# Performance work log

Hardware: AMD Instinct MI355X
Metric: run time of the kernel (lower is better)

The kernel has to match this reference:

```python
import jax, jax.numpy as jnp
import numpy as np

WIN = (8, 8)        # window height, width
HEADS = 6
DIM = 192
HEAD_DIM = DIM // HEADS
SCALE = HEAD_DIM ** -0.5
ALPHA = 0.2         # leaky_relu negative slope (tf.nn.leaky_relu / keras default)


def _leaky(t):
    return jnp.where(t >= 0, t, ALPHA * t)


def _relative_position_index():
    # Faithful to the TF code: tf.meshgrid defaults to 'xy' indexing.
    wh, ww = WIN
    mh, mw = jnp.meshgrid(jnp.arange(wh), jnp.arange(ww))  # each [ww, wh] (xy)
    coords = jnp.stack([mh, mw])                           # [2, ww, wh]
    flat = coords.reshape(2, -1)                           # [2, N]
    rel = flat[:, :, None] - flat[:, None, :]              # [2, N, N]
    rel = jnp.transpose(rel, (1, 2, 0))                    # [N, N, 2]
    idx = (rel[:, :, 0] + wh - 1) * (2 * ww - 1) + (rel[:, :, 1] + ww - 1)
    return idx                                             # [N, N] int32


def setup_inputs() -> dict:
    key = jax.random.key(0)
    ks = jax.random.split(key, 6)
    B_, N, C = 4096, WIN[0] * WIN[1], DIM
    std = 0.02
    return {
        "x": jax.random.normal(ks[0], (B_, N, C), dtype=jnp.float32),
        "wq": jax.random.normal(ks[1], (C, C), dtype=jnp.float32) * (C ** -0.5),
        "bq": jnp.zeros((C,), dtype=jnp.float32),
        "wkv": jax.random.normal(ks[2], (C, 2 * C), dtype=jnp.float32) * (C ** -0.5),
        "bkv": jnp.zeros((2 * C,), dtype=jnp.float32),
        "bias_table": jax.random.normal(ks[3], ((2 * WIN[0] - 1) * (2 * WIN[1] - 1), HEADS), dtype=jnp.float32) * std,
        "proj_w": jax.random.normal(ks[4], (C, C), dtype=jnp.float32) * (C ** -0.5),
        "proj_b": jnp.zeros((C,), dtype=jnp.float32),
    }


def reference(x, wq, bq, wkv, bkv, bias_table, proj_w, proj_b):
    B_, N, C = x.shape
    H, D = HEADS, HEAD_DIM

    # QKV projections with LeakyReLU activation (as in LinearProjection)
    q = _leaky(x @ wq + bq).reshape(B_, N, H, D).transpose(0, 2, 1, 3)      # [B,H,N,D]
    kv = _leaky(x @ wkv + bkv).reshape(B_, N, 2, H, D).transpose(2, 0, 3, 1, 4)
    k, v = kv[0], kv[1]                                                      # [B,H,N,D]

    # scaled attention scores
    attn = jnp.einsum('bhnd,bhmd->bhnm', q * SCALE, k)                       # [B,H,N,N]

    # gathered relative position bias (ratio == 1 here, tf.repeat is no-op)
    idx = _relative_position_index()                                         # [N,N]
    bias = bias_table[idx]                                                   # [N,N,H]
    attn = attn + jnp.transpose(bias, (2, 0, 1))[None]                       # [B,H,N,N]

    attn = jax.nn.softmax(attn, axis=-1)
    out = jnp.einsum('bhnm,bhmd->bhnd', attn, v)                             # [B,H,N,D]
    out = out.transpose(0, 2, 1, 3).reshape(B_, N, C)
    return out @ proj_w + proj_b
```

## Files before the change

kernel.cpp:

```cpp
#include <hip/hip_runtime.h>
#include <hip/hip_bf16.h>

typedef __bf16 bf16;
typedef bf16 bf16x8 __attribute__((ext_vector_type(8)));
typedef bf16 bf16x4 __attribute__((ext_vector_type(4)));
typedef short s16x4 __attribute__((ext_vector_type(4)));
typedef float f32x4 __attribute__((ext_vector_type(4)));

#define SCALE 0.17677669529663687f

#define XSTR 208
#define SMEM_ELEMS 13312

#if defined(__has_builtin)
#if __has_builtin(__builtin_amdgcn_mfma_f32_16x16x16bf16_1k)
#define HAS_MFMA16 1
#endif
#endif

__global__ void wattn_prep(const float* __restrict__ wq, const float* __restrict__ wkv,
                           const float* __restrict__ bias_table, const float* __restrict__ proj_w,
                           bf16* __restrict__ wqkvT, bf16* __restrict__ projT,
                           float* __restrict__ biasB)
{
    int t = blockIdx.x * 256 + threadIdx.x;
    if (t < 110592) {
        int n = t / 192, k = t % 192;
        float v = (n < 192) ? wq[k * 192 + n] : wkv[k * 384 + (n - 192)];
        wqkvT[t] = (bf16)v;
    } else if (t < 147456) {
        int e = t - 110592;
        int n = e / 192, k = e % 192;
        projT[e] = (bf16)proj_w[k * 192 + n];
    } else if (t < 172032) {
        int e = t - 147456;
        int h  = e >> 12;
        int mb = (e >> 8) & 15;
        int n  = (e >> 2) & 63;
        int mr = e & 3;
        int m  = mb * 4 + mr;
        int idx = ((n & 7) - (m & 7) + 7) * 15 + ((n >> 3) - (m >> 3) + 7);
        biasB[e] = bias_table[idx * 6 + h];
    }
}

#if !defined(HAS_MFMA16)
__device__ __forceinline__ bf16x8 build8(bf16x4 t0, bf16x4 t1, int li, int gi) {
    union { bf16x4 v; unsigned u[2]; } a0, a1;
    a0.v = t0; a1.v = t1;
    int b = li + 32 * (gi & 1);
    unsigned l0  = __shfl(a0.u[0], b),      l1  = __shfl(a0.u[1], b);
    unsigned l0h = __shfl(a0.u[0], b + 16), l1h = __shfl(a0.u[1], b + 16);
    unsigned h0  = __shfl(a1.u[0], b),      h1  = __shfl(a1.u[1], b);
    unsigned h0h = __shfl(a1.u[0], b + 16), h1h = __shfl(a1.u[1], b + 16);
    bool hi = (gi & 2);
    union { bf16x8 v8; unsigned u[4]; } r;
    r.u[0] = hi ? h0 : l0;   r.u[1] = hi ? h1 : l1;
    r.u[2] = hi ? h0h : l0h; r.u[3] = hi ? h1h : l1h;
    return r.v8;
}
#endif

__global__ __launch_bounds__(384, 4)
void wattn_main(const float* __restrict__ x, const bf16* __restrict__ wqkvT,
                const float* __restrict__ bq, const float* __restrict__ bkv,
                const bf16* __restrict__ projT, const float* __restrict__ biasB,
                const float* __restrict__ proj_b, float* __restrict__ outg)
{
    __shared__ __align__(16) bf16 smem[SMEM_ELEMS];
    const int tid = threadIdx.x;
    const int li  = tid & 15;
    const int gi  = (tid >> 4) & 3;
    const int w   = tid >> 6;
    const int win = blockIdx.x;

    bf16* xb = smem;
    const int srow = tid / 48, scol = tid % 48;
    const f32x4 fz = {0.f, 0.f, 0.f, 0.f};

    {
        const float4* xg = (const float4*)(x + (size_t)win * 12288);
#pragma unroll
        for (int i = 0; i < 8; ++i) {
            float4 p = xg[(srow + 8 * i) * 48 + scol];
            bf16x4 v; v[0]=(bf16)p.x; v[1]=(bf16)p.y; v[2]=(bf16)p.z; v[3]=(bf16)p.w;
            *(bf16x4*)&xb[(srow + 8 * i) * XSTR + scol * 4] = v;
        }
    }
    __syncthreads();

    bf16x4 qf[2][4], kf[2][4];
    {
        f32x4 bjq0 = *(const f32x4*)&bq [32 * w + 4 * gi];
        f32x4 bjq1 = *(const f32x4*)&bq [32 * w + 16 + 4 * gi];
        f32x4 bjk0 = *(const f32x4*)&bkv[32 * w + 4 * gi];
        f32x4 bjk1 = *(const f32x4*)&bkv[32 * w + 16 + 4 * gi];
        f32x4 aqk[4][4];
#pragma unroll
        for (int c = 0; c < 4; ++c) {
            aqk[0][c] = bjq0; aqk[1][c] = bjq1;
            aqk[2][c] = bjk0; aqk[3][c] = bjk1;
        }
#pragma unroll 2
        for (int kk = 0; kk < 6; ++kk) {
            bf16x8 bx[4], aw[4];
#pragma unroll
            for (int c = 0; c < 4; ++c)
                bx[c] = *(const bf16x8*)&xb[(c * 16 + li) * XSTR + kk * 32 + gi * 8];
#pragma unroll
            for (int j = 0; j < 4; ++j) {
                int T = (j < 2) ? (2 * w + j) : (12 + 2 * w + (j - 2));
                aw[j] = *(const bf16x8*)&wqkvT[(size_t)(T * 16 + li) * 192 + kk * 32 + gi * 8];
            }
#pragma unroll
            for (int j = 0; j < 4; ++j)
#pragma unroll
                for (int c = 0; c < 4; ++c)
                    aqk[j][c] = __builtin_amdgcn_mfma_f32_16x16x32_bf16(aw[j], bx[c], aqk[j][c], 0, 0, 0);
        }
#pragma unroll
        for (int j = 0; j < 2; ++j)
#pragma unroll
            for (int c = 0; c < 4; ++c) {
                bf16x4 rq, rk;
#pragma unroll
                for (int rg = 0; rg < 4; ++rg) {
                    float tq = aqk[j][c][rg];
                    float tk = aqk[2 + j][c][rg];
                    tq = (fmaxf(tq, 0.f) + 0.2f * fminf(tq, 0.f)) * SCALE;
                    tk =  fmaxf(tk, 0.f) + 0.2f * fminf(tk, 0.f);
                    rq[rg] = (bf16)tq;
                    rk[rg] = (bf16)tk;
                }
                qf[j][c] = rq;
                kf[j][c] = rk;
            }
    }

    f32x4 s[4][4];
#pragma unroll
    for (int cm = 0; cm < 4; ++cm)
#pragma unroll
        for (int cn = 0; cn < 4; ++cn) {
            f32x4 bv = *(const f32x4*)&biasB[w * 4096 + (4 * cm + gi) * 256 + (16 * cn + li) * 4];
#if defined(HAS_MFMA16)
            f32x4 t = __builtin_amdgcn_mfma_f32_16x16x16bf16_1k(
                __builtin_bit_cast(s16x4, kf[0][cm]), __builtin_bit_cast(s16x4, qf[0][cn]), bv, 0, 0, 0);
            s[cm][cn] = __builtin_amdgcn_mfma_f32_16x16x16bf16_1k(
                __builtin_bit_cast(s16x4, kf[1][cm]), __builtin_bit_cast(s16x4, qf[1][cn]), t, 0, 0, 0);
#else
            s[cm][cn] = __builtin_amdgcn_mfma_f32_16x16x32_bf16(
                build8(kf[0][cm], kf[1][cm], li, gi), build8(qf[0][cn], qf[1][cn], li, gi), bv, 0, 0, 0);
#endif
        }

    float rs[4];
    bf16x4 pb[4][4];
#pragma unroll
    for (int cn = 0; cn < 4; ++cn) {
        float m_ = -1e30f;
#pragma unroll
        for (int cm = 0; cm < 4; ++cm)
#pragma unroll
            for (int rg = 0; rg < 4; ++rg) m_ = fmaxf(m_, s[cm][cn][rg]);
        m_ = fmaxf(m_, __shfl_xor(m_, 16));
        m_ = fmaxf(m_, __shfl_xor(m_, 32));
        float ss = 0.f;
#pragma unroll
        for (int cm = 0; cm < 4; ++cm) {
            bf16x4 r;
#pragma unroll
            for (int rg = 0; rg < 4; ++rg) {
                float p = __expf(s[cm][cn][rg] - m_);
                ss += p;
                r[rg] = (bf16)p;
            }
            pb[cm][cn] = r;
        }
        ss += __shfl_xor(ss, 16);
        ss += __shfl_xor(ss, 32);
        rs[cn] = 1.f / ss;
    }

    bf16x4 vf[2][4];
    {
        f32x4 bjv0 = *(const f32x4*)&bkv[192 + 32 * w + 4 * gi];
        f32x4 bjv1 = *(const f32x4*)&bkv[192 + 32 * w + 16 + 4 * gi];
        f32x4 av_[4][2];
#pragma unroll
        for (int rt = 0; rt < 4; ++rt) { av_[rt][0] = bjv0; av_[rt][1] = bjv1; }
#pragma unroll 2
        for (int kk = 0; kk < 6; ++kk) {
            bf16x8 a[4], bwv[2];
#pragma unroll
            for (int rt = 0; rt < 4; ++rt)
                a[rt] = *(const bf16x8*)&xb[(rt * 16 + li) * XSTR + kk * 32 + gi * 8];
#pragma unroll
            for (int j = 0; j < 2; ++j)
                bwv[j] = *(const bf16x8*)&wqkvT[(size_t)((24 + 2 * w + j) * 16 + li) * 192 + kk * 32 + gi * 8];
#pragma unroll
            for (int rt = 0; rt < 4; ++rt)
#pragma unroll
                for (int j = 0; j < 2; ++j)
                    av_[rt][j] = __builtin_amdgcn_mfma_f32_16x16x32_bf16(a[rt], bwv[j], av_[rt][j], 0, 0, 0);
        }
#pragma unroll
        for (int j = 0; j < 2; ++j)
#pragma unroll
            for (int rt = 0; rt < 4; ++rt) {
                bf16x4 r;
#pragma unroll
                for (int rg = 0; rg < 4; ++rg) {
                    float t = av_[rt][j][rg];
                    t = fmaxf(t, 0.f) + 0.2f * fminf(t, 0.f);
                    r[rg] = (bf16)t;
                }
                vf[j][rt] = r;
            }
    }

    f32x4 o[2][4];
#pragma unroll
    for (int ct = 0; ct < 2; ++ct)
#pragma unroll
        for (int cn = 0; cn < 4; ++cn) {
#if defined(HAS_MFMA16)
            f32x4 t = fz;
#pragma unroll
            for (int rt = 0; rt < 4; ++rt)
                t = __builtin_amdgcn_mfma_f32_16x16x16bf16_1k(
                        __builtin_bit_cast(s16x4, vf[ct][rt]),
                        __builtin_bit_cast(s16x4, pb[rt][cn]), t, 0, 0, 0);
            o[ct][cn] = t;
#else
            f32x4 t = fz;
#pragma unroll
            for (int c = 0; c < 2; ++c)
                t = __builtin_amdgcn_mfma_f32_16x16x32_bf16(
                        build8(vf[ct][2 * c], vf[ct][2 * c + 1], li, gi),
                        build8(pb[2 * c][cn], pb[2 * c + 1][cn], li, gi), t, 0, 0, 0);
            o[ct][cn] = t;
#endif
        }
    __syncthreads();

#pragma unroll
    for (int ct = 0; ct < 2; ++ct)
#pragma unroll
        for (int cn = 0; cn < 4; ++cn) {
            bf16x4 r;
#pragma unroll
            for (int rg = 0; rg < 4; ++rg) r[rg] = (bf16)(o[ct][cn][rg] * rs[cn]);
            *(bf16x4*)&xb[(cn * 16 + li) * XSTR + 32 * w + 16 * ct + 4 * gi] = r;
        }
    __syncthreads();

    f32x4 pa[2][4];
    {
        f32x4 pb0 = *(const f32x4*)&proj_b[32 * w + 4 * gi];
        f32x4 pb1 = *(const f32x4*)&proj_b[32 * w + 16 + 4 * gi];
#pragma unroll
        for (int cn = 0; cn < 4; ++cn) { pa[0][cn] = pb0; pa[1][cn] = pb1; }
    }
#pragma unroll 2
    for (int kk = 0; kk < 6; ++kk) {
        bf16x8 bo[4], awp[2];
#pragma unroll
        for (int cn = 0; cn < 4; ++cn)
            bo[cn] = *(const bf16x8*)&xb[(cn * 16 + li) * XSTR + kk * 32 + gi * 8];
#pragma unroll
        for (int ct = 0; ct < 2; ++ct)
            awp[ct] = *(const bf16x8*)&projT[(size_t)((2 * w + ct) * 16 + li) * 192 + kk * 32 + gi * 8];
#pragma unroll
        for (int ct = 0; ct < 2; ++ct)
#pragma unroll
            for (int cn = 0; cn < 4; ++cn)
                pa[ct][cn] = __builtin_amdgcn_mfma_f32_16x16x32_bf16(awp[ct], bo[cn], pa[ct][cn], 0, 0, 0);
    }

    {
        const int L = tid & 63;
        const int src = (L >> 2) + 16 * (L & 3);
        f32x4* og = (f32x4*)(outg + (size_t)win * 12288);
#pragma unroll
        for (int cn = 0; cn < 4; ++cn)
#pragma unroll
            for (int ct = 0; ct < 2; ++ct) {
                f32x4 y;
#pragma unroll
                for (int e = 0; e < 4; ++e)
                    y[e] = __shfl(pa[ct][cn][e], src);
                og[(16 * cn + (L >> 2)) * 48 + 8 * w + 4 * ct + (L & 3)] = y;
            }
    }
}

extern "C" void kernel_launch(void* const* d_in, const int* in_sizes, int n_in,
                              void* d_out, int out_size, void* d_ws, size_t ws_size,
                              hipStream_t stream)
{
    const float* x          = (const float*)d_in[0];
    const float* wq         = (const float*)d_in[1];
    const float* bq         = (const float*)d_in[2];
    const float* wkv        = (const float*)d_in[3];
    const float* bkv        = (const float*)d_in[4];
    const float* bias_table = (const float*)d_in[5];
    const float* proj_w     = (const float*)d_in[6];
    const float* proj_b     = (const float*)d_in[7];
    float* out = (float*)d_out;

    int B = in_sizes[0] / (64 * 192);

    bf16*  wqkvT = (bf16*)d_ws;
    bf16*  projT = (bf16*)((char*)d_ws + 221184);
    float* biasB = (float*)((char*)d_ws + 294912);

    wattn_prep<<<672, 256, 0, stream>>>(wq, wkv, bias_table, proj_w, wqkvT, projT, biasB);

    wattn_main<<<B, 384, 0, stream>>>(x, wqkvT, bq, bkv, projT, biasB, proj_b, out);
}
```

Before: 241.8 us.

## Process two windows per block with double-buffered x prefetch and MFMA priority

```diff
diff --git a/kernel.cpp b/kernel.cpp
--- a/kernel.cpp
+++ b/kernel.cpp
@@ -10,7 +10,8 @@
 #define SCALE 0.17677669529663687f
 
 #define XSTR 208
-#define SMEM_ELEMS 13312
+#define XELEMS 13312
+#define SMEM_ELEMS 26624
 
 #if defined(__has_builtin)
 #if __has_builtin(__builtin_amdgcn_mfma_f32_16x16x16bf16_1k)
@@ -65,233 +66,270 @@
 void wattn_main(const float* __restrict__ x, const bf16* __restrict__ wqkvT,
                 const float* __restrict__ bq, const float* __restrict__ bkv,
                 const bf16* __restrict__ projT, const float* __restrict__ biasB,
-                const float* __restrict__ proj_b, float* __restrict__ outg)
+                const float* __restrict__ proj_b, float* __restrict__ outg, int B)
 {
     __shared__ __align__(16) bf16 smem[SMEM_ELEMS];
     const int tid = threadIdx.x;
     const int li  = tid & 15;
     const int gi  = (tid >> 4) & 3;
     const int w   = tid >> 6;
-    const int win = blockIdx.x;
-
-    bf16* xb = smem;
+    const int win0 = blockIdx.x * 2;
+    if (win0 >= B) return;
+
     const int srow = tid / 48, scol = tid % 48;
     const f32x4 fz = {0.f, 0.f, 0.f, 0.f};
 
     {
-        const float4* xg = (const float4*)(x + (size_t)win * 12288);
-#pragma unroll
-        for (int i = 0; i < 8; ++i) {
-            float4 p = xg[(srow + 8 * i) * 48 + scol];
+        const float4* xg = (const float4*)(x + (size_t)win0 * 12288);
+#pragma unroll
+        for (int t = 0; t < 8; ++t) {
+            float4 p = xg[(srow + 8 * t) * 48 + scol];
             bf16x4 v; v[0]=(bf16)p.x; v[1]=(bf16)p.y; v[2]=(bf16)p.z; v[3]=(bf16)p.w;
-            *(bf16x4*)&xb[(srow + 8 * i) * XSTR + scol * 4] = v;
+            *(bf16x4*)&smem[(srow + 8 * t) * XSTR + scol * 4] = v;
         }
     }
     __syncthreads();
 
-    bf16x4 qf[2][4], kf[2][4];
-    {
-        f32x4 bjq0 = *(const f32x4*)&bq [32 * w + 4 * gi];
-        f32x4 bjq1 = *(const f32x4*)&bq [32 * w + 16 + 4 * gi];
-        f32x4 bjk0 = *(const f32x4*)&bkv[32 * w + 4 * gi];
-        f32x4 bjk1 = *(const f32x4*)&bkv[32 * w + 16 + 4 * gi];
-        f32x4 aqk[4][4];
-#pragma unroll
-        for (int c = 0; c < 4; ++c) {
-            aqk[0][c] = bjq0; aqk[1][c] = bjq1;
-            aqk[2][c] = bjk0; aqk[3][c] = bjk1;
-        }
+    int cur = 0;
+#pragma unroll 1
+    for (int i = 0; i < 2; ++i) {
+        const int win = win0 + i;
+        if (win >= B) break;
+        bf16* xb = smem + cur * XELEMS;
+        const bool pf = (i == 0) && (win0 + 1 < B);
+
+        bf16x4 qf[2][4], kf[2][4];
+        {
+            f32x4 bjq0 = *(const f32x4*)&bq [32 * w + 4 * gi];
+            f32x4 bjq1 = *(const f32x4*)&bq [32 * w + 16 + 4 * gi];
+            f32x4 bjk0 = *(const f32x4*)&bkv[32 * w + 4 * gi];
+            f32x4 bjk1 = *(const f32x4*)&bkv[32 * w + 16 + 4 * gi];
+            f32x4 aqk[4][4];
+#pragma unroll
+            for (int c = 0; c < 4; ++c) {
+                aqk[0][c] = bjq0; aqk[1][c] = bjq1;
+                aqk[2][c] = bjk0; aqk[3][c] = bjk1;
+            }
+            __builtin_amdgcn_s_setprio(1);
+#pragma unroll 2
+            for (int kk = 0; kk < 6; ++kk) {
+                bf16x8 bx[4], aw[4];
+#pragma unroll
+                for (int c = 0; c < 4; ++c)
+                    bx[c] = *(const bf16x8*)&xb[(c * 16 + li) * XSTR + kk * 32 + gi * 8];
+#pragma unroll
+                for (int j = 0; j < 4; ++j) {
+                    int T = (j < 2) ? (2 * w + j) : (12 + 2 * w + (j - 2));
+                    aw[j] = *(const bf16x8*)&wqkvT[(size_t)(T * 16 + li) * 192 + kk * 32 + gi * 8];
+                }
+#pragma unroll
+                for (int j = 0; j < 4; ++j)
+#pragma unroll
+                    for (int c = 0; c < 4; ++c)
+                        aqk[j][c] = __builtin_amdgcn_mfma_f32_16x16x32_bf16(aw[j], bx[c], aqk[j][c], 0, 0, 0);
+            }
+            __builtin_amdgcn_s_setprio(0);
+#pragma unroll
+            for (int j = 0; j < 2; ++j)
+#pragma unroll
+                for (int c = 0; c < 4; ++c) {
+                    bf16x4 rq, rk;
+#pragma unroll
+                    for (int rg = 0; rg < 4; ++rg) {
+                        float tq = aqk[j][c][rg];
+                        float tk = aqk[2 + j][c][rg];
+                        tq = (fmaxf(tq, 0.f) + 0.2f * fminf(tq, 0.f)) * SCALE;
+                        tk =  fmaxf(tk, 0.f) + 0.2f * fminf(tk, 0.f);
+                        rq[rg] = (bf16)tq;
+                        rk[rg] = (bf16)tk;
+                    }
+                    qf[j][c] = rq;
+                    kf[j][c] = rk;
+                }
+        }
+
+        f32x4 s[4][4];
+        __builtin_amdgcn_s_setprio(1);
+#pragma unroll
+        for (int cm = 0; cm < 4; ++cm)
+#pragma unroll
+            for (int cn = 0; cn < 4; ++cn) {
+                f32x4 bv = *(const f32x4*)&biasB[w * 4096 + (4 * cm + gi) * 256 + (16 * cn + li) * 4];
+#if defined(HAS_MFMA16)
+                f32x4 t = __builtin_amdgcn_mfma_f32_16x16x16bf16_1k(
+                    __builtin_bit_cast(s16x4, kf[0][cm]), __builtin_bit_cast(s16x4, qf[0][cn]), bv, 0, 0, 0);
+                s[cm][cn] = __builtin_amdgcn_mfma_f32_16x16x16bf16_1k(
+                    __builtin_bit_cast(s16x4, kf[1][cm]), __builtin_bit_cast(s16x4, qf[1][cn]), t, 0, 0, 0);
+#else
+                s[cm][cn] = __builtin_amdgcn_mfma_f32_16x16x32_bf16(
+                    build8(kf[0][cm], kf[1][cm], li, gi), build8(qf[0][cn], qf[1][cn], li, gi), bv, 0, 0, 0);
+#endif
+            }
+        __builtin_amdgcn_s_setprio(0);
+
+        float rs[4];
+        bf16x4 pb[4][4];
+#pragma unroll
+        for (int cn = 0; cn < 4; ++cn) {
+            float m_ = -1e30f;
+#pragma unroll
+            for (int cm = 0; cm < 4; ++cm)
+#pragma unroll
+                for (int rg = 0; rg < 4; ++rg) m_ = fmaxf(m_, s[cm][cn][rg]);
+            m_ = fmaxf(m_, __shfl_xor(m_, 16));
+            m_ = fmaxf(m_, __shfl_xor(m_, 32));
+            float ss = 0.f;
+#pragma unroll
+            for (int cm = 0; cm < 4; ++cm) {
+                bf16x4 r;
+#pragma unroll
+                for (int rg = 0; rg < 4; ++rg) {
+                    float p = __expf(s[cm][cn][rg] - m_);
+                    ss += p;
+                    r[rg] = (bf16)p;
+                }
+                pb[cm][cn] = r;
+            }
+            ss += __shfl_xor(ss, 16);
+            ss += __shfl_xor(ss, 32);
+            rs[cn] = 1.f / ss;
+        }
+
+        bf16x4 vf[2][4];
+        {
+            f32x4 bjv0 = *(const f32x4*)&bkv[192 + 32 * w + 4 * gi];
+            f32x4 bjv1 = *(const f32x4*)&bkv[192 + 32 * w + 16 + 4 * gi];
+            f32x4 av_[4][2];
+#pragma unroll
+            for (int rt = 0; rt < 4; ++rt) { av_[rt][0] = bjv0; av_[rt][1] = bjv1; }
+            __builtin_amdgcn_s_setprio(1);
+#pragma unroll 2
+            for (int kk = 0; kk < 6; ++kk) {
+                bf16x8 a[4], bwv[2];
+#pragma unroll
+                for (int rt = 0; rt < 4; ++rt)
+                    a[rt] = *(const bf16x8*)&xb[(rt * 16 + li) * XSTR + kk * 32 + gi * 8];
+#pragma unroll
+                for (int j = 0; j < 2; ++j)
+                    bwv[j] = *(const bf16x8*)&wqkvT[(size_t)((24 + 2 * w + j) * 16 + li) * 192 + kk * 32 + gi * 8];
+#pragma unroll
+                for (int rt = 0; rt < 4; ++rt)
+#pragma unroll
+                    for (int j = 0; j < 2; ++j)
+                        av_[rt][j] = __builtin_amdgcn_mfma_f32_16x16x32_bf16(a[rt], bwv[j], av_[rt][j], 0, 0, 0);
+            }
+            __builtin_amdgcn_s_setprio(0);
+#pragma unroll
+            for (int j = 0; j < 2; ++j)
+#pragma unroll
+                for (int rt = 0; rt < 4; ++rt) {
+                    bf16x4 r;
+#pragma unroll
+                    for (int rg = 0; rg < 4; ++rg) {
+                        float t = av_[rt][j][rg];
+                        t = fmaxf(t, 0.f) + 0.2f * fminf(t, 0.f);
+                        r[rg] = (bf16)t;
+                    }
+                    vf[j][rt] = r;
+                }
+        }
+
+        float4 px[8];
+        if (pf) {
+            const float4* xg2 = (const float4*)(x + (size_t)(win + 1) * 12288);
+#pragma unroll
+            for (int t = 0; t < 8; ++t) px[t] = xg2[(srow + 8 * t) * 48 + scol];
+        }
+
+        bf16x4 obf[2][4];
+        __builtin_amdgcn_s_setprio(1);
+#pragma unroll
+        for (int ct = 0; ct < 2; ++ct)
+#pragma unroll
+            for (int cn = 0; cn < 4; ++cn) {
+#if defined(HAS_MFMA16)
+                f32x4 t = fz;
+#pragma unroll
+                for (int rt = 0; rt < 4; ++rt)
+                    t = __builtin_amdgcn_mfma_f32_16x16x16bf16_1k(
+                            __builtin_bit_cast(s16x4, vf[ct][rt]),
+                            __builtin_bit_cast(s16x4, pb[rt][cn]), t, 0, 0, 0);
+#else
+                f32x4 t = fz;
+#pragma unroll
+                for (int c = 0; c < 2; ++c)
+                    t = __builtin_amdgcn_mfma_f32_16x16x32_bf16(
+                            build8(vf[ct][2 * c], vf[ct][2 * c + 1], li, gi),
+                            build8(pb[2 * c][cn], pb[2 * c + 1][cn], li, gi), t, 0, 0, 0);
+#endif
+                bf16x4 r;
+#pragma unroll
+                for (int rg = 0; rg < 4; ++rg) r[rg] = (bf16)(t[rg] * rs[cn]);
+                obf[ct][cn] = r;
+            }
+        __builtin_amdgcn_s_setprio(0);
+        __syncthreads();
+
+#pragma unroll
+        for (int ct = 0; ct < 2; ++ct)
+#pragma unroll
+            for (int cn = 0; cn < 4; ++cn)
+                *(bf16x4*)&xb[(cn * 16 + li) * XSTR + 32 * w + 16 * ct + 4 * gi] = obf[ct][cn];
+        if (pf) {
+            bf16* xn = smem + (cur ^ 1) * XELEMS;
+#pragma unroll
+            for (int t = 0; t < 8; ++t) {
+                bf16x4 v; v[0]=(bf16)px[t].x; v[1]=(bf16)px[t].y; v[2]=(bf16)px[t].z; v[3]=(bf16)px[t].w;
+                *(bf16x4*)&xn[(srow + 8 * t) * XSTR + scol * 4] = v;
+            }
+        }
+        __syncthreads();
+
+        f32x4 pa[2][4];
+        {
+            f32x4 pb0 = *(const f32x4*)&proj_b[32 * w + 4 * gi];
+            f32x4 pb1 = *(const f32x4*)&proj_b[32 * w + 16 + 4 * gi];
+#pragma unroll
+            for (int cn = 0; cn < 4; ++cn) { pa[0][cn] = pb0; pa[1][cn] = pb1; }
+        }
+        __builtin_amdgcn_s_setprio(1);
 #pragma unroll 2
         for (int kk = 0; kk < 6; ++kk) {
-            bf16x8 bx[4], aw[4];
-#pragma unroll
-            for (int c = 0; c < 4; ++c)
-                bx[c] = *(const bf16x8*)&xb[(c * 16 + li) * XSTR + kk * 32 + gi * 8];
-#pragma unroll
-            for (int j = 0; j < 4; ++j) {
-                int T = (j < 2) ? (2 * w + j) : (12 + 2 * w + (j - 2));
-                aw[j] = *(const bf16x8*)&wqkvT[(size_t)(T * 16 + li) * 192 + kk * 32 + gi * 8];
-            }
-#pragma unroll
-            for (int j = 0; j < 4; ++j)
-#pragma unroll
-                for (int c = 0; c < 4; ++c)
-                    aqk[j][c] = __builtin_amdgcn_mfma_f32_16x16x32_bf16(aw[j], bx[c], aqk[j][c], 0, 0, 0);
-        }
-#pragma unroll
-        for (int j = 0; j < 2; ++j)
-#pragma unroll
-            for (int c = 0; c < 4; ++c) {
-                bf16x4 rq, rk;
-#pragma unroll
-                for (int rg = 0; rg < 4; ++rg) {
-                    float tq = aqk[j][c][rg];
-                    float tk = aqk[2 + j][c][rg];
-                    tq = (fmaxf(tq, 0.f) + 0.2f * fminf(tq, 0.f)) * SCALE;
-                    tk =  fmaxf(tk, 0.f) + 0.2f * fminf(tk, 0.f);
-                    rq[rg] = (bf16)tq;
-                    rk[rg] = (bf16)tk;
-                }
-                qf[j][c] = rq;
-                kf[j][c] = rk;
-            }
-    }
-
-    f32x4 s[4][4];
-#pragma unroll
-    for (int cm = 0; cm < 4; ++cm)
-#pragma unroll
-        for (int cn = 0; cn < 4; ++cn) {
-            f32x4 bv = *(const f32x4*)&biasB[w * 4096 + (4 * cm + gi) * 256 + (16 * cn + li) * 4];
-#if defined(HAS_MFMA16)
-            f32x4 t = __builtin_amdgcn_mfma_f32_16x16x16bf16_1k(
-                __builtin_bit_cast(s16x4, kf[0][cm]), __builtin_bit_cast(s16x4, qf[0][cn]), bv, 0, 0, 0);
-            s[cm][cn] = __builtin_amdgcn_mfma_f32_16x16x16bf16_1k(
-                __builtin_bit_cast(s16x4, kf[1][cm]), __builtin_bit_cast(s16x4, qf[1][cn]), t, 0, 0, 0);
-#else
-            s[cm][cn] = __builtin_amdgcn_mfma_f32_16x16x32_bf16(
-                build8(kf[0][cm], kf[1][cm], li, gi), build8(qf[0][cn], qf[1][cn], li, gi), bv, 0, 0, 0);
-#endif
-        }
-
-    float rs[4];
-    bf16x4 pb[4][4];
-#pragma unroll
-    for (int cn = 0; cn < 4; ++cn) {
-        float m_ = -1e30f;
-#pragma unroll
-        for (int cm = 0; cm < 4; ++cm)
-#pragma unroll
-            for (int rg = 0; rg < 4; ++rg) m_ = fmaxf(m_, s[cm][cn][rg]);
-        m_ = fmaxf(m_, __shfl_xor(m_, 16));
-        m_ = fmaxf(m_, __shfl_xor(m_, 32));
-        float ss = 0.f;
-#pragma unroll
-        for (int cm = 0; cm < 4; ++cm) {
-            bf16x4 r;
-#pragma unroll
-            for (int rg = 0; rg < 4; ++rg) {
-                float p = __expf(s[cm][cn][rg] - m_);
-                ss += p;
-                r[rg] = (bf16)p;
-            }
-            pb[cm][cn] = r;
-        }
-        ss += __shfl_xor(ss, 16);
-        ss += __shfl_xor(ss, 32);
-        rs[cn] = 1.f / ss;
-    }
-
-    bf16x4 vf[2][4];
-    {
-        f32x4 bjv0 = *(const f32x4*)&bkv[192 + 32 * w + 4 * gi];
-        f32x4 bjv1 = *(const f32x4*)&bkv[192 + 32 * w + 16 + 4 * gi];
-        f32x4 av_[4][2];
-#pragma unroll
-        for (int rt = 0; rt < 4; ++rt) { av_[rt][0] = bjv0; av_[rt][1] = bjv1; }
-#pragma unroll 2
-        for (int kk = 0; kk < 6; ++kk) {
-            bf16x8 a[4], bwv[2];
-#pragma unroll
-            for (int rt = 0; rt < 4; ++rt)
-                a[rt] = *(const bf16x8*)&xb[(rt * 16 + li) * XSTR + kk * 32 + gi * 8];
-#pragma unroll
-            for (int j = 0; j < 2; ++j)
-                bwv[j] = *(const bf16x8*)&wqkvT[(size_t)((24 + 2 * w + j) * 16 + li) * 192 + kk * 32 + gi * 8];
-#pragma unroll
-            for (int rt = 0; rt < 4; ++rt)
-#pragma unroll
-                for (int j = 0; j < 2; ++j)
-                    av_[rt][j] = __builtin_amdgcn_mfma_f32_16x16x32_bf16(a[rt], bwv[j], av_[rt][j], 0, 0, 0);
-        }
-#pragma unroll
-        for (int j = 0; j < 2; ++j)
-#pragma unroll
-            for (int rt = 0; rt < 4; ++rt) {
-                bf16x4 r;
-#pragma unroll
-                for (int rg = 0; rg < 4; ++rg) {
-                    float t = av_[rt][j][rg];
-                    t = fmaxf(t, 0.f) + 0.2f * fminf(t, 0.f);
-                    r[rg] = (bf16)t;
-                }
-                vf[j][rt] = r;
-            }
-    }
-
-    f32x4 o[2][4];
-#pragma unroll
-    for (int ct = 0; ct < 2; ++ct)
-#pragma unroll
-        for (int cn = 0; cn < 4; ++cn) {
-#if defined(HAS_MFMA16)
-            f32x4 t = fz;
-#pragma unroll
-            for (int rt = 0; rt < 4; ++rt)
-                t = __builtin_amdgcn_mfma_f32_16x16x16bf16_1k(
-                        __builtin_bit_cast(s16x4, vf[ct][rt]),
-                        __builtin_bit_cast(s16x4, pb[rt][cn]), t, 0, 0, 0);
-            o[ct][cn] = t;
-#else
-            f32x4 t = fz;
-#pragma unroll
-            for (int c = 0; c < 2; ++c)
-                t = __builtin_amdgcn_mfma_f32_16x16x32_bf16(
-                        build8(vf[ct][2 * c], vf[ct][2 * c + 1], li, gi),
-                        build8(pb[2 * c][cn], pb[2 * c + 1][cn], li, gi), t, 0, 0, 0);
-            o[ct][cn] = t;
-#endif
-        }
-    __syncthreads();
-
-#pragma unroll
-    for (int ct = 0; ct < 2; ++ct)
-#pragma unroll
-        for (int cn = 0; cn < 4; ++cn) {
-            bf16x4 r;
-#pragma unroll
-            for (int rg = 0; rg < 4; ++rg) r[rg] = (bf16)(o[ct][cn][rg] * rs[cn]);
-            *(bf16x4*)&xb[(cn * 16 + li) * XSTR + 32 * w + 16 * ct + 4 * gi] = r;
-        }
-    __syncthreads();
-
-    f32x4 pa[2][4];
-    {
-        f32x4 pb0 = *(const f32x4*)&proj_b[32 * w + 4 * gi];
-        f32x4 pb1 = *(const f32x4*)&proj_b[32 * w + 16 + 4 * gi];
-#pragma unroll
-        for (int cn = 0; cn < 4; ++cn) { pa[0][cn] = pb0; pa[1][cn] = pb1; }
-    }
-#pragma unroll 2
-    for (int kk = 0; kk < 6; ++kk) {
-        bf16x8 bo[4], awp[2];
-#pragma unroll
-        for (int cn = 0; cn < 4; ++cn)
-            bo[cn] = *(const bf16x8*)&xb[(cn * 16 + li) * XSTR + kk * 32 + gi * 8];
-#pragma unroll
-        for (int ct = 0; ct < 2; ++ct)
-            awp[ct] = *(const bf16x8*)&projT[(size_t)((2 * w + ct) * 16 + li) * 192 + kk * 32 + gi * 8];
-#pragma unroll
-        for (int ct = 0; ct < 2; ++ct)
+            bf16x8 bo[4], awp[2];
 #pragma unroll
             for (int cn = 0; cn < 4; ++cn)
-                pa[ct][cn] = __builtin_amdgcn_mfma_f32_16x16x32_bf16(awp[ct], bo[cn], pa[ct][cn], 0, 0, 0);
-    }
-
-    {
-        const int L = tid & 63;
-        const int src = (L >> 2) + 16 * (L & 3);
-        f32x4* og = (f32x4*)(outg + (size_t)win * 12288);
-#pragma unroll
-        for (int cn = 0; cn < 4; ++cn)
-#pragma unroll
-            for (int ct = 0; ct < 2; ++ct) {
-                f32x4 y;
-#pragma unroll
-                for (int e = 0; e < 4; ++e)
-                    y[e] = __shfl(pa[ct][cn][e], src);
-                og[(16 * cn + (L >> 2)) * 48 + 8 * w + 4 * ct + (L & 3)] = y;
-            }
+                bo[cn] = *(const bf16x8*)&xb[(cn * 16 + li) * XSTR + kk * 32 + gi * 8];
+#pragma unroll
+            for (int ct = 0; ct < 2; ++ct)
+                awp[ct] = *(const bf16x8*)&projT[(size_t)((2 * w + ct) * 16 + li) * 192 + kk * 32 + gi * 8];
+#pragma unroll
+            for (int ct = 0; ct < 2; ++ct)
+#pragma unroll
+                for (int cn = 0; cn < 4; ++cn)
+                    pa[ct][cn] = __builtin_amdgcn_mfma_f32_16x16x32_bf16(awp[ct], bo[cn], pa[ct][cn], 0, 0, 0);
+        }
+        __builtin_amdgcn_s_setprio(0);
+
+        {
+            const int L = tid & 63;
+            f32x4* og = (f32x4*)(outg + (size_t)win * 12288);
+#pragma unroll
+            for (int cn = 0; cn < 4; ++cn)
+#pragma unroll
+                for (int h = 0; h < 2; ++h) {
+                    const int sl = 8 * h + (L >> 3) + 16 * (L & 3);
+                    f32x4 y;
+#pragma unroll
+                    for (int e = 0; e < 4; ++e) {
+                        float v0 = __shfl(pa[0][cn][e], sl);
+                        float v1 = __shfl(pa[1][cn][e], sl);
+                        y[e] = (L & 4) ? v1 : v0;
+                    }
+                    og[(16 * cn + 8 * h + (L >> 3)) * 48 + 8 * w + (L & 7)] = y;
+                }
+        }
+
+        cur ^= 1;
     }
 }
 
@@ -317,5 +355,5 @@
 
     wattn_prep<<<672, 256, 0, stream>>>(wq, wkv, bias_table, proj_w, wqkvT, projT, biasB);
 
-    wattn_main<<<B, 384, 0, stream>>>(x, wqkvT, bq, bkv, projT, biasB, proj_b, out);
+    wattn_main<<<(B + 1) / 2, 384, 0, stream>>>(x, wqkvT, bq, bkv, projT, biasB, proj_b, out, B);
 }
```

Result: slower. 503.5 us (+108.2%).
